# Optimization experiments

Hardware: AMD Instinct MI355X
Metric: run time of the kernel (lower is better)

## Reference

```python
import jax, jax.numpy as jnp
import numpy as np

# Static config mirroring SlidingGaussianWindow1d(minTP=256, wsize=32)
MINTP = 256
WSIZE = 32
NWIN = MINTP - WSIZE  # 224 sliding windows
_nT = MINTP if MINTP % 2 == 0 else MINTP + 1
_m = _nT // 2                      # gaussian center
_w = int(np.round(WSIZE / 2))      # half box width

# box window b and sharp gaussian gw_init (buffers in the torch module)
_b_np = np.zeros(_nT, dtype=np.float32)
_b_np[_m - _w:_m + _w] = 1.0
_B = jnp.asarray(_b_np)
_GW_INIT = jnp.exp(-(jnp.arange(_nT, dtype=jnp.float32) - _m) ** 2)

# The torch loop rolls Ashift cumulatively: at window ii the total roll is
# -sum_{k<=ii} s_k with s_k = round(-minTP/2) + round(wsize/2) + k + 1.
# roll(A, -S)[t] == A[(t + S) % T], so precompute a gather index table.
_S = np.cumsum([int(np.round(-MINTP / 2) + np.round(WSIZE / 2) + k + 1)
                for k in range(NWIN)])
_IDX = jnp.asarray((np.arange(MINTP)[None, :] + _S[:, None]) % MINTP)  # (Nwin, T)


def _window_weights(win_alpha):
    # gw = gw_init / (2*alpha^2); smoothed box via full convolution, then
    # peak-normalized and cropped to length minTP (as in the torch forward).
    gw = _GW_INIT / (2.0 * win_alpha[0] * win_alpha[0])
    A = jnp.convolve(gw, _B)                 # length 2*nT - 1
    A = A / A.max()
    A = A[_m:A.shape[0] - _m + 1][:MINTP]    # length minTP
    return A[_IDX]                           # (Nwin, T) all rolled windows


def _forward(x, win_alpha):
    W = _window_weights(win_alpha)                      # (Nwin, T)
    tc = x[:, None, :, :] * W[None, :, :, None]         # (B, Nwin, T, C)
    tc = tc - tc.mean(axis=2, keepdims=True)            # center over time
    cov = jnp.einsum('bwtc,bwtd->bwcd', tc, tc) / (MINTP - 1)
    d = jnp.sqrt(jnp.diagonal(cov, axis1=-2, axis2=-1))  # (B, Nwin, C)
    corr = cov / (d[..., :, None] * d[..., None, :])
    return jnp.clip(corr, -1.0, 1.0)                    # torch.corrcoef clamps


def setup_inputs() -> dict:
    key = jax.random.key(0)
    x = jax.random.normal(key, (16, MINTP, 64), dtype=jnp.float32)
    win_alpha = jnp.full((1,), 0.5, dtype=jnp.float32)
    return {"x": x, "win_alpha": win_alpha}


def reference(x, win_alpha):
    return _forward(x, win_alpha)
```

## Files before the change

### kernel.cpp

```cpp
#include <hip/hip_runtime.h>
#include <hip/hip_bf16.h>


static constexpr int TT   = 256;
static constexpr int CC   = 64;
static constexpr int NW   = 224;
static constexpr int KS   = 64;
static constexpr int U0   = 96;
static constexpr int KPAD = KS + 8;

typedef short bf16x8 __attribute__((ext_vector_type(8)));
typedef float f32x16 __attribute__((ext_vector_type(16)));

__global__ __launch_bounds__(256) void corr_kernel(const float* __restrict__ x,
                                                   const float* __restrict__ alpha,
                                                   float* __restrict__ out) {
    __shared__ float Ed[32];
    __shared__ float Wn[KS];
    __shared__ __align__(16) __hip_bfloat16 Yt[CC][KPAD];
    __shared__ float red[4][CC];
    __shared__ float colsum[CC];
    __shared__ float rdiag[CC];

    const int tid = threadIdx.x;
    const int blk = blockIdx.x;
    const int b = blk / NW;
    const int w = blk - b * NW;
    const int S = ((w + 1) * (w - 222)) / 2;

    if (tid < 25) {
        float a = alpha[0];
        float scale = 1.0f / (2.0f * a * a);
        float d = (float)(tid - 12);
        Ed[tid] = expf(-d * d) * scale;
    }
    __syncthreads();
    if (tid < KS) {
        float tot = 0.f;
        for (int k = 0; k < 25; ++k) tot += Ed[k];
        int t = U0 + tid;
        int dlo = t - 143, dhi = t - 112;
        if (dlo < -12) dlo = -12;
        if (dhi > 12) dhi = 12;
        float s = 0.f;
        for (int d = dlo; d <= dhi; ++d) s += Ed[d + 12];
        Wn[tid] = s / tot;
    }
    __syncthreads();

    const float* xb = x + (size_t)b * TT * CC;
    const int c = tid & 63;
    const int q = tid >> 6;
    float csum = 0.f;
#pragma unroll
    for (int it = 0; it < (KS >> 3); ++it) {
        int uu = it * 8 + q * 2;
        int t0 = (U0 + uu - S) & 255;
        int t1 = (U0 + uu + 1 - S) & 255;
        float v0 = xb[t0 * CC + c] * Wn[uu];
        float v1 = xb[t1 * CC + c] * Wn[uu + 1];
        __hip_bfloat16 h0 = __float2bfloat16(v0);
        __hip_bfloat16 h1 = __float2bfloat16(v1);
        csum += __bfloat162float(h0) + __bfloat162float(h1);
        unsigned short us0 = *(unsigned short*)&h0;
        unsigned short us1 = *(unsigned short*)&h1;
        unsigned pk = ((unsigned)us1 << 16) | (unsigned)us0;
        *(unsigned*)&Yt[c][uu] = pk;
    }
    red[q][c] = csum;
    __syncthreads();
    if (tid < CC) colsum[tid] = red[0][tid] + red[1][tid] + red[2][tid] + red[3][tid];

    const int wv = tid >> 6;
    const int lane = tid & 63;
    const int ti = wv >> 1, tj = wv & 1;
    const int r32 = lane & 31, half = lane >> 5;
    f32x16 acc;
#pragma unroll
    for (int i = 0; i < 16; ++i) acc[i] = 0.f;
    const __hip_bfloat16* arow = &Yt[32 * ti + r32][half * 8];
    const __hip_bfloat16* brow = &Yt[32 * tj + r32][half * 8];
#pragma unroll
    for (int k0 = 0; k0 < KS; k0 += 16) {
        bf16x8 af = *(const bf16x8*)(arow + k0);
        bf16x8 bf = *(const bf16x8*)(brow + k0);
        acc = __builtin_amdgcn_mfma_f32_32x32x16_bf16(af, bf, acc, 0, 0, 0);
    }
    __syncthreads();

    constexpr float invT  = 1.0f / 256.0f;
    constexpr float invT1 = 1.0f / 255.0f;
    if (ti == tj) {
        int needHalf = (r32 >> 2) & 1;
        if (half == needHalf) {
            int reg = ((r32 >> 3) << 2) | (r32 & 3);
            float g = acc[0];
#pragma unroll
            for (int rr = 1; rr < 16; ++rr)
                if (rr == reg) g = acc[rr];
            int cg = 32 * ti + r32;
            float mu = colsum[cg] * invT;
            float cv = (g - 256.0f * mu * mu) * invT1;
            rdiag[cg] = rsqrtf(fmaxf(cv, 1e-38f));
        }
    }
    __syncthreads();

    float* outb = out + (size_t)blk * (CC * CC);
#pragma unroll
    for (int rr = 0; rr < 16; ++rr) {
        int row = 32 * ti + (rr & 3) + 8 * (rr >> 2) + 4 * half;
        int col = 32 * tj + r32;
        float mur = colsum[row] * invT;
        float muc = colsum[col] * invT;
        float cv = (acc[rr] - 256.0f * mur * muc) * invT1;
        float cr = cv * rdiag[row] * rdiag[col];
        cr = fminf(1.0f, fmaxf(-1.0f, cr));
        outb[row * CC + col] = cr;
    }
}

extern "C" void kernel_launch(void* const* d_in, const int* in_sizes, int n_in,
                              void* d_out, int out_size, void* d_ws, size_t ws_size,
                              hipStream_t stream) {
    const float* x     = (const float*)d_in[0];
    const float* alpha = (const float*)d_in[1];
    float* out = (float*)d_out;
    (void)d_ws; (void)ws_size;

    corr_kernel<<<16 * NW, 256, 0, stream>>>(x, alpha, out);
}
```

Measured before the change: 79.30 us.

## Precompute window weights at compile time, vectorize loads, and swizzle LDS layout

```diff
diff --git a/kernel.cpp b/kernel.cpp
--- a/kernel.cpp
+++ b/kernel.cpp
@@ -5,20 +5,41 @@
 static constexpr int TT   = 256;
 static constexpr int CC   = 64;
 static constexpr int NW   = 224;
-static constexpr int KS   = 64;
 static constexpr int U0   = 96;
-static constexpr int KPAD = KS + 8;
+static constexpr int KPAD = 72;
+static constexpr int PSTR = 68;
 
 typedef short bf16x8 __attribute__((ext_vector_type(8)));
 typedef float f32x16 __attribute__((ext_vector_type(16)));
 
-__global__ __launch_bounds__(256) void corr_kernel(const float* __restrict__ x,
-                                                   const float* __restrict__ alpha,
-                                                   float* __restrict__ out) {
-    __shared__ float Ed[32];
-    __shared__ float Wn[KS];
+static constexpr float EXPT[13] = {
+    1.0f, 3.67879441e-1f, 1.83156389e-2f, 1.23409804e-4f,
+    1.12535175e-7f, 1.38879439e-11f, 2.31952283e-16f, 5.24288566e-22f,
+    1.60381089e-28f, 6.63700000e-36f, 0.0f, 0.0f, 0.0f };
+
+struct alignas(16) WTab { float w[64]; };
+
+static constexpr WTab make_wtab() {
+    WTab t{};
+    float tot = 0.f;
+    for (int d = -12; d <= 12; ++d) tot += EXPT[d < 0 ? -d : d];
+    for (int u = 0; u < 64; ++u) {
+        int tc = U0 + u;
+        int dlo = tc - 143; if (dlo < -12) dlo = -12;
+        int dhi = tc - 112; if (dhi > 12)  dhi = 12;
+        float s = 0.f;
+        for (int d = dlo; d <= dhi; ++d) s += EXPT[d < 0 ? -d : d];
+        t.w[u] = s / tot;
+    }
+    return t;
+}
+__device__ constexpr WTab WTAB = make_wtab();
+
+__global__ __launch_bounds__(256, 8) void corr_kernel(const float* __restrict__ x,
+                                                      const float* __restrict__ alpha,
+                                                      float* __restrict__ out) {
     __shared__ __align__(16) __hip_bfloat16 Yt[CC][KPAD];
-    __shared__ float red[4][CC];
+    __shared__ __align__(16) float Pred[16][PSTR];
     __shared__ float colsum[CC];
     __shared__ float rdiag[CC];
 
@@ -28,93 +49,101 @@
     const int w = blk - b * NW;
     const int S = ((w + 1) * (w - 222)) / 2;
 
-    if (tid < 25) {
-        float a = alpha[0];
-        float scale = 1.0f / (2.0f * a * a);
-        float d = (float)(tid - 12);
-        Ed[tid] = expf(-d * d) * scale;
+    float aa = alpha[0]; aa = aa * aa;
+    const float f = aa / aa;
+
+    const int g   = tid >> 4;
+    const int a   = tid & 15;
+    const int c4  = a << 2;
+    const int swz = (a & 7) << 3;
+
+    const float2* W2 = (const float2*)WTAB.w;
+    float2 wlo = W2[g];
+    float2 whi = W2[g + 16];
+    wlo.x *= f; wlo.y *= f; whi.x *= f; whi.y *= f;
+
+    const float* xb = x + (size_t)b * (TT * CC);
+    float ps[4] = {0.f, 0.f, 0.f, 0.f};
+#pragma unroll
+    for (int p = 0; p < 2; ++p) {
+        const int u0 = 32 * p + 2 * g;
+        const int t0 = (U0 + u0 - S) & 255;
+        const int t1 = (U0 + u0 + 1 - S) & 255;
+        const float4 v0 = *(const float4*)(xb + t0 * CC + c4);
+        const float4 v1 = *(const float4*)(xb + t1 * CC + c4);
+        const float wa = p ? whi.x : wlo.x;
+        const float wb = p ? whi.y : wlo.y;
+        const int uc = u0 ^ swz;
+        const float e0[4] = {v0.x, v0.y, v0.z, v0.w};
+        const float e1[4] = {v1.x, v1.y, v1.z, v1.w};
+#pragma unroll
+        for (int i = 0; i < 4; ++i) {
+            __hip_bfloat16 h0 = __float2bfloat16(e0[i] * wa);
+            __hip_bfloat16 h1 = __float2bfloat16(e1[i] * wb);
+            ps[i] += __bfloat162float(h0) + __bfloat162float(h1);
+            unsigned pk = ((unsigned)*(unsigned short*)&h1 << 16) |
+                          (unsigned)*(unsigned short*)&h0;
+            *(unsigned*)&Yt[c4 + i][uc] = pk;
+        }
     }
-    __syncthreads();
-    if (tid < KS) {
-        float tot = 0.f;
-        for (int k = 0; k < 25; ++k) tot += Ed[k];
-        int t = U0 + tid;
-        int dlo = t - 143, dhi = t - 112;
-        if (dlo < -12) dlo = -12;
-        if (dhi > 12) dhi = 12;
-        float s = 0.f;
-        for (int d = dlo; d <= dhi; ++d) s += Ed[d + 12];
-        Wn[tid] = s / tot;
+    {
+        float4 psv = {ps[0], ps[1], ps[2], ps[3]};
+        *(float4*)&Pred[g][c4] = psv;
     }
     __syncthreads();
 
-    const float* xb = x + (size_t)b * TT * CC;
-    const int c = tid & 63;
-    const int q = tid >> 6;
-    float csum = 0.f;
-#pragma unroll
-    for (int it = 0; it < (KS >> 3); ++it) {
-        int uu = it * 8 + q * 2;
-        int t0 = (U0 + uu - S) & 255;
-        int t1 = (U0 + uu + 1 - S) & 255;
-        float v0 = xb[t0 * CC + c] * Wn[uu];
-        float v1 = xb[t1 * CC + c] * Wn[uu + 1];
-        __hip_bfloat16 h0 = __float2bfloat16(v0);
-        __hip_bfloat16 h1 = __float2bfloat16(v1);
-        csum += __bfloat162float(h0) + __bfloat162float(h1);
-        unsigned short us0 = *(unsigned short*)&h0;
-        unsigned short us1 = *(unsigned short*)&h1;
-        unsigned pk = ((unsigned)us1 << 16) | (unsigned)us0;
-        *(unsigned*)&Yt[c][uu] = pk;
-    }
-    red[q][c] = csum;
-    __syncthreads();
-    if (tid < CC) colsum[tid] = red[0][tid] + red[1][tid] + red[2][tid] + red[3][tid];
-
-    const int wv = tid >> 6;
-    const int lane = tid & 63;
+    const int wv = tid >> 6, lane = tid & 63;
     const int ti = wv >> 1, tj = wv & 1;
     const int r32 = lane & 31, half = lane >> 5;
+    const int sg = (r32 >> 2) & 7;
+
     f32x16 acc;
 #pragma unroll
     for (int i = 0; i < 16; ++i) acc[i] = 0.f;
-    const __hip_bfloat16* arow = &Yt[32 * ti + r32][half * 8];
-    const __hip_bfloat16* brow = &Yt[32 * tj + r32][half * 8];
+    const __hip_bfloat16* ya = &Yt[32 * ti + r32][0];
+    const __hip_bfloat16* yb = &Yt[32 * tj + r32][0];
 #pragma unroll
-    for (int k0 = 0; k0 < KS; k0 += 16) {
-        bf16x8 af = *(const bf16x8*)(arow + k0);
-        bf16x8 bf = *(const bf16x8*)(brow + k0);
+    for (int t = 0; t < 4; ++t) {
+        const int off = ((2 * t + half) ^ sg) << 3;
+        bf16x8 af = *(const bf16x8*)(ya + off);
+        bf16x8 bf = *(const bf16x8*)(yb + off);
         acc = __builtin_amdgcn_mfma_f32_32x32x16_bf16(af, bf, acc, 0, 0, 0);
+    }
+
+    if (tid < CC) {
+        float s = 0.f;
+#pragma unroll
+        for (int gg = 0; gg < 16; ++gg) s += Pred[gg][tid];
+        colsum[tid] = s;
     }
     __syncthreads();
 
-    constexpr float invT  = 1.0f / 256.0f;
-    constexpr float invT1 = 1.0f / 255.0f;
+    constexpr float invT = 1.0f / 256.0f;
     if (ti == tj) {
-        int needHalf = (r32 >> 2) & 1;
+        const int needHalf = (r32 >> 2) & 1;
         if (half == needHalf) {
-            int reg = ((r32 >> 3) << 2) | (r32 & 3);
-            float g = acc[0];
+            const int reg = ((r32 >> 3) << 2) | (r32 & 3);
+            float gd = acc[0];
 #pragma unroll
             for (int rr = 1; rr < 16; ++rr)
-                if (rr == reg) g = acc[rr];
-            int cg = 32 * ti + r32;
-            float mu = colsum[cg] * invT;
-            float cv = (g - 256.0f * mu * mu) * invT1;
-            rdiag[cg] = rsqrtf(fmaxf(cv, 1e-38f));
+                if (rr == reg) gd = acc[rr];
+            const int cg = 32 * ti + r32;
+            const float cs = colsum[cg];
+            const float raw = gd - cs * cs * invT;
+            rdiag[cg] = rsqrtf(fmaxf(raw, 1e-36f));
         }
     }
     __syncthreads();
 
     float* outb = out + (size_t)blk * (CC * CC);
+    const int col = 32 * tj + r32;
+    const float qc  = colsum[col] * invT;
+    const float rdc = rdiag[col];
 #pragma unroll
     for (int rr = 0; rr < 16; ++rr) {
-        int row = 32 * ti + (rr & 3) + 8 * (rr >> 2) + 4 * half;
-        int col = 32 * tj + r32;
-        float mur = colsum[row] * invT;
-        float muc = colsum[col] * invT;
-        float cv = (acc[rr] - 256.0f * mur * muc) * invT1;
-        float cr = cv * rdiag[row] * rdiag[col];
+        const int row = 32 * ti + (rr & 3) + 8 * (rr >> 2) + 4 * half;
+        const float cv = acc[rr] - colsum[row] * qc;
+        float cr = cv * rdiag[row] * rdc;
         cr = fminf(1.0f, fmaxf(-1.0f, cr));
         outb[row * CC + col] = cr;
     }
```

Result: no change. 78.10 us, median of 2 (-1.5%).
